# Kernel tuning notes

Hardware: AMD Instinct MI355X
Metric: run time of the kernel (lower is better)

## Reference

```python
import jax, jax.numpy as jnp
import numpy as np

DELTA = 10.0
EPS = 1e-08
THRESHOLD = 0.9
STEEPNESS = 10.0


def setup_inputs() -> dict:
    key = jax.random.key(0)
    k1, k2 = jax.random.split(key)
    B, T2, T1, F = 16, 2048, 512, 128
    mels = jax.random.normal(k1, (B, T2, F), dtype=jnp.float32)
    alpha = jax.random.uniform(k2, (B, T2, T1), dtype=jnp.float32)
    mel_mask = jnp.ones((B, T2), dtype=jnp.int32)
    text_mask = jnp.ones((B, T1), dtype=jnp.int32)
    return {"mels": mels, "alpha": alpha, "mel_mask": mel_mask, "text_mask": text_mask}


def reference(mels, alpha, mel_mask, text_mask):
    B, T2, F = mels.shape
    T1 = text_mask.shape[-1]
    audio_mask = mel_mask.astype(bool)
    txt_mask = text_mask.astype(bool)
    am_f = audio_mask.astype(alpha.dtype)  # [B, T2]
    tm_f = txt_mask.astype(alpha.dtype)    # [B, T1]

    # index vector p: [B, T1]
    p = jnp.broadcast_to(jnp.arange(T1, dtype=alpha.dtype), (B, T1))

    # cosine similarity between consecutive frames (F.normalize: x / max(||x||, 1e-12))
    norm = jnp.maximum(jnp.linalg.norm(mels, axis=-1, keepdims=True), 1e-12)
    z_norm = mels / norm
    cosine_sim = jnp.sum(z_norm[:, :-1] * z_norm[:, 1:], axis=-1)  # [B, T2-1]
    activity = jax.nn.sigmoid(STEEPNESS * (THRESHOLD - cosine_sim))
    activity = jnp.concatenate([jnp.ones((B, 1), dtype=activity.dtype), activity], axis=-1)
    activity = activity * am_f

    # soft monotonic index via gated cumsum of alpha-proposal increments
    imv_proposal = jnp.einsum('bts,bs->bt', alpha, p)  # [B, T2]
    delta_prop = jnp.concatenate(
        [jnp.zeros((B, 1), dtype=imv_proposal.dtype), jnp.diff(imv_proposal, axis=-1)], axis=-1)
    eff_delta = jnp.clip(delta_prop * activity, 0.0, 1.0)
    imv = jnp.cumsum(eff_delta, axis=-1) * am_f

    # rescale so last valid frame maps to last phoneme index
    last_idx = jnp.maximum(audio_mask.sum(-1).astype(jnp.int32) - 1, 0)  # [B]
    last_val = jnp.maximum(jnp.take_along_axis(imv, last_idx[:, None], axis=1)[:, 0], 1e-06)
    text_len = txt_mask.sum(-1).astype(imv.dtype)
    scale = jnp.maximum(text_len - 1.0, 0.0) / last_val
    imv = imv * scale[:, None] * am_f

    # gamma: masked softmax over phonemes of -delta * (imv - p)^2
    dist_sq = (imv[:, :, None] - p[:, None, :]) ** 2  # [B, T2, T1]
    logits = jnp.where(txt_mask[:, None, :], -DELTA * dist_sq, -1e9)
    gamma = jax.nn.softmax(logits, axis=-1) * am_f[:, :, None]

    # durations: soft mass per phoneme
    durations = jnp.sum(gamma * am_f[:, :, None], axis=1) * tm_f  # [B, T1]

    # attention-pooling of mel frames onto phonemes
    w = jnp.swapaxes(gamma, 1, 2) * am_f[:, None, :]  # [B, T1, T2]
    w = w / (jnp.sum(w, axis=-1, keepdims=True) + EPS)
    aligned_mels = jnp.einsum('bst,btf->bsf', w, mels) * tm_f[:, :, None]  # [B, T1, F]
    return aligned_mels, durations, imv
```

## Files before the change

kernel.cpp:

```cpp
#include <hip/hip_runtime.h>
#include <math.h>
#include <cstddef>

#define B_  16
#define T2_ 2048
#define T1_ 512
#define F_  128

constexpr float DELTA_C  = 10.0f;
constexpr float EPS_C    = 1e-8f;
constexpr float THRESH_C = 0.9f;
constexpr float STEEP_C  = 10.0f;

typedef float f4v __attribute__((ext_vector_type(4)));

__global__ __launch_bounds__(256) void actprop_kernel(const float* __restrict__ mels,
                                                      const float* __restrict__ alpha,
                                                      const int* __restrict__ mel_mask,
                                                      float* __restrict__ act,
                                                      float* __restrict__ prop) {
    int wid  = (int)((blockIdx.x * blockDim.x + threadIdx.x) >> 6);
    int lane = threadIdx.x & 63;
    if (wid >= B_ * T2_) return;
    int t = wid % T2_;

    const f4v* row = (const f4v*)(alpha + (size_t)wid * T1_);
    f4v v0 = __builtin_nontemporal_load(&row[lane]);
    f4v v1 = __builtin_nontemporal_load(&row[lane + 64]);

    float d = 0.f, n0 = 0.f, n1 = 0.f;
    if (t > 0) {
        float2 x = ((const float2*)(mels + (size_t)(wid - 1) * F_))[lane];
        float2 y = ((const float2*)(mels + (size_t)wid * F_))[lane];
        d  = x.x * y.x + x.y * y.y;
        n0 = x.x * x.x + x.y * x.y;
        n1 = y.x * y.x + y.y * y.y;
    }

    float fL = (float)(lane * 4);
    float psum = v0.x * fL + v0.y * (fL + 1.f) + v0.z * (fL + 2.f) + v0.w * (fL + 3.f)
               + v1.x * (fL + 256.f) + v1.y * (fL + 257.f) + v1.z * (fL + 258.f) + v1.w * (fL + 259.f);

    for (int off = 32; off > 0; off >>= 1) {
        psum += __shfl_xor(psum, off, 64);
        d    += __shfl_xor(d,    off, 64);
        n0   += __shfl_xor(n0,   off, 64);
        n1   += __shfl_xor(n1,   off, 64);
    }

    if (lane == 0) {
        float a_val;
        if (t == 0) {
            a_val = 1.0f;
        } else {
            float cs = d / (fmaxf(sqrtf(n0), 1e-12f) * fmaxf(sqrtf(n1), 1e-12f));
            a_val = 1.0f / (1.0f + __expf(-STEEP_C * (THRESH_C - cs)));
        }
        act[wid]  = a_val * (float)mel_mask[wid];
        prop[wid] = psum;
    }
}

__global__ __launch_bounds__(256) void scan_kernel(const float* __restrict__ prop,
                                                   const float* __restrict__ act,
                                                   const int* __restrict__ mel_mask,
                                                   const int* __restrict__ text_mask,
                                                   float* __restrict__ imv_out,
                                                   float2* __restrict__ packed,
                                                   int2* __restrict__ bounds) {
    int b    = blockIdx.x;
    int tid  = threadIdx.x;
    int wave = tid >> 6, lane = tid & 63;
    __shared__ float s_imv[T2_];
    __shared__ float s_wsum[4];
    __shared__ int   s_am4[4], s_tm4[4];
    __shared__ int   s_tm[T1_];

    const float* pr = prop + (size_t)b * T2_;
    const float* ac = act  + (size_t)b * T2_;
    const int*   mm = mel_mask  + (size_t)b * T2_;
    const int*   tm = text_mask + (size_t)b * T1_;

    int tmv0 = tm[tid], tmv1 = tm[tid + 256];
    s_tm[tid] = tmv0; s_tm[tid + 256] = tmv1;

    float e[8];
    int   mmv[8];
    int t0 = tid * 8;
    int am_local = 0;
    float run = 0.0f;
    for (int i = 0; i < 8; i++) {
        int t = t0 + i;
        float d = (t == 0) ? 0.0f : (pr[t] - pr[t - 1]) * ac[t];
        d = fminf(fmaxf(d, 0.0f), 1.0f);
        run += d;
        e[i] = run;
        mmv[i] = mm[t];
        am_local += mmv[i];
    }
    int tm_local = tmv0 + tmv1;
    for (int off = 32; off > 0; off >>= 1) {
        am_local += __shfl_xor(am_local, off, 64);
        tm_local += __shfl_xor(tm_local, off, 64);
    }
    if (lane == 0) { s_am4[wave] = am_local; s_tm4[wave] = tm_local; }

    float v = run;
    for (int off = 1; off < 64; off <<= 1) {
        float u = __shfl_up(v, off, 64);
        if (lane >= off) v += u;
    }
    if (lane == 63) s_wsum[wave] = v;
    __syncthreads();

    float woff = 0.0f;
    for (int w = 0; w < 4; w++) woff += (w < wave) ? s_wsum[w] : 0.0f;
    float excl = woff + v - run;
    for (int i = 0; i < 8; i++) {
        int t = t0 + i;
        s_imv[t] = (e[i] + excl) * (float)mmv[i];
    }
    __syncthreads();

    int am_total = s_am4[0] + s_am4[1] + s_am4[2] + s_am4[3];
    int tm_total = s_tm4[0] + s_tm4[1] + s_tm4[2] + s_tm4[3];
    int last_idx = max(am_total - 1, 0);
    float last_val = fmaxf(s_imv[last_idx], 1e-6f);
    float scale = fmaxf((float)tm_total - 1.0f, 0.0f) / last_val;
    __syncthreads();

    for (int i = 0; i < 8; i++) {
        int t = t0 + i;
        int valid = mmv[i];
        float vv = s_imv[t] * scale * (float)valid;
        imv_out[(size_t)b * T2_ + t] = vv;
        int c = (int)floorf(vv);
        float Z = 0.0f;
        for (int s = c - 2; s <= c + 3; s++) {
            if (s >= 0 && s < T1_ && s_tm[s]) {
                float dd = vv - (float)s;
                Z += __expf(-DELTA_C * dd * dd);
            }
        }
        Z = fmaxf(Z, 1e-30f);
        float key = valid ? vv : 3.0e4f;
        float2 pk = {key, valid ? (1.0f / Z) : 0.0f};
        packed[(size_t)b * T2_ + t] = pk;
        s_imv[t] = key;
    }
    __syncthreads();

    for (int k = 0; k < 2; k++) {
        int s = tid + k * 256;
        float lov = (float)s - 3.0f, hiv = (float)s + 3.0f;
        int lo = 0, hi = T2_;
        while (lo < hi) { int mid = (lo + hi) >> 1; if (s_imv[mid] >= lov) hi = mid; else lo = mid + 1; }
        int st = lo;
        hi = T2_;
        while (lo < hi) { int mid = (lo + hi) >> 1; if (s_imv[mid] > hiv) hi = mid; else lo = mid + 1; }
        int2 be = {st, lo};
        bounds[(size_t)b * T1_ + s] = be;
    }
}

__global__ __launch_bounds__(256) void pool_kernel(const float* __restrict__ mels,
                                                   const int* __restrict__ text_mask,
                                                   const float2* __restrict__ packed,
                                                   const int2* __restrict__ bounds,
                                                   float* __restrict__ aligned,
                                                   float* __restrict__ dur) {
    int wid  = (int)((blockIdx.x * blockDim.x + threadIdx.x) >> 6);
    int lane = threadIdx.x & 63;
    if (wid >= B_ * (T1_ / 2)) return;
    int b = wid >> 8, s0 = (wid & 255) * 2;
    float fs0 = (float)s0, fs1 = fs0 + 1.0f;

    const float2* pk   = packed + (size_t)b * T2_;
    const float2* mel2 = (const float2*)(mels + (size_t)b * T2_ * F_);
    int2 b0 = bounds[(size_t)b * T1_ + s0];
    int2 b1 = bounds[(size_t)b * T1_ + s0 + 1];
    int t_lo = b0.x, t_hi = b1.y;

    float ax0 = 0.f, ay0 = 0.f, g0s = 0.f;
    float ax1 = 0.f, ay1 = 0.f, g1s = 0.f;
    int t = t_lo;
    for (; t + 2 <= t_hi; t += 2) {
        float2 p0 = pk[t], p1 = pk[t + 1];
        float2 m0 = mel2[(size_t)t * 64 + lane];
        float2 m1 = mel2[(size_t)(t + 1) * 64 + lane];
        float d00 = p0.x - fs0, d01 = p0.x - fs1;
        float d10 = p1.x - fs0, d11 = p1.x - fs1;
        float g00 = __expf(-DELTA_C * d00 * d00) * p0.y;
        float g01 = __expf(-DELTA_C * d01 * d01) * p0.y;
        float g10 = __expf(-DELTA_C * d10 * d10) * p1.y;
        float g11 = __expf(-DELTA_C * d11 * d11) * p1.y;
        g0s += g00 + g10; g1s += g01 + g11;
        ax0 += g00 * m0.x + g10 * m1.x;  ay0 += g00 * m0.y + g10 * m1.y;
        ax1 += g01 * m0.x + g11 * m1.x;  ay1 += g01 * m0.y + g11 * m1.y;
    }
    for (; t < t_hi; t++) {
        float2 p = pk[t];
        float2 m = mel2[(size_t)t * 64 + lane];
        float d0 = p.x - fs0, d1 = p.x - fs1;
        float ga = __expf(-DELTA_C * d0 * d0) * p.y;
        float gb = __expf(-DELTA_C * d1 * d1) * p.y;
        g0s += ga; g1s += gb;
        ax0 += ga * m.x; ay0 += ga * m.y;
        ax1 += gb * m.x; ay1 += gb * m.y;
    }

    float tm0 = (float)text_mask[(size_t)b * T1_ + s0];
    float tm1 = (float)text_mask[(size_t)b * T1_ + s0 + 1];
    float inv0 = tm0 / (g0s + EPS_C);
    float inv1 = tm1 / (g1s + EPS_C);
    float2 o0 = {ax0 * inv0, ay0 * inv0};
    float2 o1 = {ax1 * inv1, ay1 * inv1};
    ((float2*)(aligned + ((size_t)b * T1_ + s0) * F_))[lane] = o0;
    ((float2*)(aligned + ((size_t)b * T1_ + s0 + 1) * F_))[lane] = o1;
    if (lane == 0) {
        dur[(size_t)b * T1_ + s0]     = g0s * tm0;
        dur[(size_t)b * T1_ + s0 + 1] = g1s * tm1;
    }
}

extern "C" void kernel_launch(void* const* d_in, const int* in_sizes, int n_in,
                              void* d_out, int out_size, void* d_ws, size_t ws_size,
                              hipStream_t stream) {
    const float* mels      = (const float*)d_in[0];
    const float* alpha     = (const float*)d_in[1];
    const int*   mel_mask  = (const int*)d_in[2];
    const int*   text_mask = (const int*)d_in[3];

    float* out     = (float*)d_out;
    float* aligned = out;
    float* dur     = out + (size_t)B_ * T1_ * F_;
    float* imv     = dur + (size_t)B_ * T1_;

    float*  ws     = (float*)d_ws;
    float*  act    = ws;
    float*  prop   = ws + (size_t)B_ * T2_;
    float2* packed = (float2*)(ws + 2 * (size_t)B_ * T2_);
    int2*   bounds = (int2*)(ws + 4 * (size_t)B_ * T2_);

    dim3 blk(256);
    actprop_kernel<<<(B_ * T2_) / 4, blk, 0, stream>>>(mels, alpha, mel_mask, act, prop);
    scan_kernel   <<<B_,            blk, 0, stream>>>(prop, act, mel_mask, text_mask, imv, packed, bounds);
    pool_kernel   <<<(B_ * T1_ / 2) / 4, blk, 0, stream>>>(mels, text_mask, packed, bounds, aligned, dur);
}
```

Before: 133.1 us.

## Fuse scan into pool kernel with redundant per-block scan recomputation

Merges the per-batch scan kernel into the pooling kernel: each of 64 blocks per batch recomputes the cumsum, scale and normalizers into shared memory, then pools 8 phonemes. This removes one launch, the 16-block serial scan stage and the global packed/bounds round trip. Act and prop are also packed into one float2 workspace array. The cost is 64x redundant scan work per batch and larger shared memory use.

New measurement: 134.4 us. Within noise of the previous version (+1.0%).

```diff
diff --git a/kernel.cpp b/kernel.cpp
--- a/kernel.cpp
+++ b/kernel.cpp
@@ -17,8 +17,7 @@
 __global__ __launch_bounds__(256) void actprop_kernel(const float* __restrict__ mels,
                                                       const float* __restrict__ alpha,
                                                       const int* __restrict__ mel_mask,
-                                                      float* __restrict__ act,
-                                                      float* __restrict__ prop) {
+                                                      float2* __restrict__ pa) {
     int wid  = (int)((blockIdx.x * blockDim.x + threadIdx.x) >> 6);
     int lane = threadIdx.x & 63;
     if (wid >= B_ * T2_) return;
@@ -56,30 +55,32 @@
             float cs = d / (fmaxf(sqrtf(n0), 1e-12f) * fmaxf(sqrtf(n1), 1e-12f));
             a_val = 1.0f / (1.0f + __expf(-STEEP_C * (THRESH_C - cs)));
         }
-        act[wid]  = a_val * (float)mel_mask[wid];
-        prop[wid] = psum;
+        float2 o = {psum, a_val * (float)mel_mask[wid]};
+        pa[wid] = o;
     }
 }
 
-__global__ __launch_bounds__(256) void scan_kernel(const float* __restrict__ prop,
-                                                   const float* __restrict__ act,
+__global__ __launch_bounds__(256) void pool_kernel(const float* __restrict__ mels,
+                                                   const float2* __restrict__ pa,
                                                    const int* __restrict__ mel_mask,
                                                    const int* __restrict__ text_mask,
                                                    float* __restrict__ imv_out,
-                                                   float2* __restrict__ packed,
-                                                   int2* __restrict__ bounds) {
-    int b    = blockIdx.x;
+                                                   float* __restrict__ aligned,
+                                                   float* __restrict__ dur) {
+    int bi   = blockIdx.x;
+    int b    = bi >> 6, sblk = bi & 63;
     int tid  = threadIdx.x;
     int wave = tid >> 6, lane = tid & 63;
-    __shared__ float s_imv[T2_];
+
+    __shared__ float s_key[T2_];
+    __shared__ float s_r[T2_];
     __shared__ float s_wsum[4];
     __shared__ int   s_am4[4], s_tm4[4];
     __shared__ int   s_tm[T1_];
 
-    const float* pr = prop + (size_t)b * T2_;
-    const float* ac = act  + (size_t)b * T2_;
-    const int*   mm = mel_mask  + (size_t)b * T2_;
-    const int*   tm = text_mask + (size_t)b * T1_;
+    const float2* pr = pa + (size_t)b * T2_;
+    const int*    mm = mel_mask  + (size_t)b * T2_;
+    const int*    tm = text_mask + (size_t)b * T1_;
 
     int tmv0 = tm[tid], tmv1 = tm[tid + 256];
     s_tm[tid] = tmv0; s_tm[tid + 256] = tmv1;
@@ -87,11 +88,14 @@
     float e[8];
     int   mmv[8];
     int t0 = tid * 8;
+    float prev = (t0 > 0) ? pr[t0 - 1].x : 0.0f;
+    float run = 0.0f;
     int am_local = 0;
-    float run = 0.0f;
     for (int i = 0; i < 8; i++) {
         int t = t0 + i;
-        float d = (t == 0) ? 0.0f : (pr[t] - pr[t - 1]) * ac[t];
+        float2 cur = pr[t];
+        float d = (t == 0) ? 0.0f : (cur.x - prev) * cur.y;
+        prev = cur.x;
         d = fminf(fmaxf(d, 0.0f), 1.0f);
         run += d;
         e[i] = run;
@@ -118,22 +122,22 @@
     float excl = woff + v - run;
     for (int i = 0; i < 8; i++) {
         int t = t0 + i;
-        s_imv[t] = (e[i] + excl) * (float)mmv[i];
+        s_key[t] = (e[i] + excl) * (float)mmv[i];
     }
     __syncthreads();
 
     int am_total = s_am4[0] + s_am4[1] + s_am4[2] + s_am4[3];
     int tm_total = s_tm4[0] + s_tm4[1] + s_tm4[2] + s_tm4[3];
     int last_idx = max(am_total - 1, 0);
-    float last_val = fmaxf(s_imv[last_idx], 1e-6f);
+    float last_val = fmaxf(s_key[last_idx], 1e-6f);
     float scale = fmaxf((float)tm_total - 1.0f, 0.0f) / last_val;
     __syncthreads();
 
     for (int i = 0; i < 8; i++) {
         int t = t0 + i;
         int valid = mmv[i];
-        float vv = s_imv[t] * scale * (float)valid;
-        imv_out[(size_t)b * T2_ + t] = vv;
+        float vv = s_key[t] * scale * (float)valid;
+        if (sblk == 0) imv_out[(size_t)b * T2_ + t] = vv;
         int c = (int)floorf(vv);
         float Z = 0.0f;
         for (int s = c - 2; s <= c + 3; s++) {
@@ -143,74 +147,54 @@
             }
         }
         Z = fmaxf(Z, 1e-30f);
-        float key = valid ? vv : 3.0e4f;
-        float2 pk = {key, valid ? (1.0f / Z) : 0.0f};
-        packed[(size_t)b * T2_ + t] = pk;
-        s_imv[t] = key;
-    }
-    __syncthreads();
-
-    for (int k = 0; k < 2; k++) {
-        int s = tid + k * 256;
-        float lov = (float)s - 3.0f, hiv = (float)s + 3.0f;
-        int lo = 0, hi = T2_;
-        while (lo < hi) { int mid = (lo + hi) >> 1; if (s_imv[mid] >= lov) hi = mid; else lo = mid + 1; }
-        int st = lo;
-        hi = T2_;
-        while (lo < hi) { int mid = (lo + hi) >> 1; if (s_imv[mid] > hiv) hi = mid; else lo = mid + 1; }
-        int2 be = {st, lo};
-        bounds[(size_t)b * T1_ + s] = be;
-    }
-}
-
-__global__ __launch_bounds__(256) void pool_kernel(const float* __restrict__ mels,
-                                                   const int* __restrict__ text_mask,
-                                                   const float2* __restrict__ packed,
-                                                   const int2* __restrict__ bounds,
-                                                   float* __restrict__ aligned,
-                                                   float* __restrict__ dur) {
-    int wid  = (int)((blockIdx.x * blockDim.x + threadIdx.x) >> 6);
-    int lane = threadIdx.x & 63;
-    if (wid >= B_ * (T1_ / 2)) return;
-    int b = wid >> 8, s0 = (wid & 255) * 2;
+        s_key[t] = valid ? vv : 3.0e4f;
+        s_r[t]   = valid ? (1.0f / Z) : 0.0f;
+    }
+    __syncthreads();
+
+    int s0 = sblk * 8 + wave * 2;
     float fs0 = (float)s0, fs1 = fs0 + 1.0f;
-
-    const float2* pk   = packed + (size_t)b * T2_;
     const float2* mel2 = (const float2*)(mels + (size_t)b * T2_ * F_);
-    int2 b0 = bounds[(size_t)b * T1_ + s0];
-    int2 b1 = bounds[(size_t)b * T1_ + s0 + 1];
-    int t_lo = b0.x, t_hi = b1.y;
+
+    float lov = fs0 - 3.0f, hiv = fs1 + 3.0f;
+    int lo = 0, hi = T2_;
+    while (lo < hi) { int mid = (lo + hi) >> 1; if (s_key[mid] >= lov) hi = mid; else lo = mid + 1; }
+    int t_lo = lo;
+    hi = T2_;
+    while (lo < hi) { int mid = (lo + hi) >> 1; if (s_key[mid] > hiv) hi = mid; else lo = mid + 1; }
+    int t_hi = lo;
 
     float ax0 = 0.f, ay0 = 0.f, g0s = 0.f;
     float ax1 = 0.f, ay1 = 0.f, g1s = 0.f;
     int t = t_lo;
     for (; t + 2 <= t_hi; t += 2) {
-        float2 p0 = pk[t], p1 = pk[t + 1];
+        float k0 = s_key[t], r0 = s_r[t];
+        float k1 = s_key[t + 1], r1 = s_r[t + 1];
         float2 m0 = mel2[(size_t)t * 64 + lane];
         float2 m1 = mel2[(size_t)(t + 1) * 64 + lane];
-        float d00 = p0.x - fs0, d01 = p0.x - fs1;
-        float d10 = p1.x - fs0, d11 = p1.x - fs1;
-        float g00 = __expf(-DELTA_C * d00 * d00) * p0.y;
-        float g01 = __expf(-DELTA_C * d01 * d01) * p0.y;
-        float g10 = __expf(-DELTA_C * d10 * d10) * p1.y;
-        float g11 = __expf(-DELTA_C * d11 * d11) * p1.y;
+        float d00 = k0 - fs0, d01 = k0 - fs1;
+        float d10 = k1 - fs0, d11 = k1 - fs1;
+        float g00 = __expf(-DELTA_C * d00 * d00) * r0;
+        float g01 = __expf(-DELTA_C * d01 * d01) * r0;
+        float g10 = __expf(-DELTA_C * d10 * d10) * r1;
+        float g11 = __expf(-DELTA_C * d11 * d11) * r1;
         g0s += g00 + g10; g1s += g01 + g11;
         ax0 += g00 * m0.x + g10 * m1.x;  ay0 += g00 * m0.y + g10 * m1.y;
         ax1 += g01 * m0.x + g11 * m1.x;  ay1 += g01 * m0.y + g11 * m1.y;
     }
     for (; t < t_hi; t++) {
-        float2 p = pk[t];
+        float k = s_key[t], r = s_r[t];
         float2 m = mel2[(size_t)t * 64 + lane];
-        float d0 = p.x - fs0, d1 = p.x - fs1;
-        float ga = __expf(-DELTA_C * d0 * d0) * p.y;
-        float gb = __expf(-DELTA_C * d1 * d1) * p.y;
+        float d0 = k - fs0, d1 = k - fs1;
+        float ga = __expf(-DELTA_C * d0 * d0) * r;
+        float gb = __expf(-DELTA_C * d1 * d1) * r;
         g0s += ga; g1s += gb;
         ax0 += ga * m.x; ay0 += ga * m.y;
         ax1 += gb * m.x; ay1 += gb * m.y;
     }
 
-    float tm0 = (float)text_mask[(size_t)b * T1_ + s0];
-    float tm1 = (float)text_mask[(size_t)b * T1_ + s0 + 1];
+    float tm0 = (float)s_tm[s0];
+    float tm1 = (float)s_tm[s0 + 1];
     float inv0 = tm0 / (g0s + EPS_C);
     float inv1 = tm1 / (g1s + EPS_C);
     float2 o0 = {ax0 * inv0, ay0 * inv0};
@@ -236,14 +220,9 @@
     float* dur     = out + (size_t)B_ * T1_ * F_;
     float* imv     = dur + (size_t)B_ * T1_;
 
-    float*  ws     = (float*)d_ws;
-    float*  act    = ws;
-    float*  prop   = ws + (size_t)B_ * T2_;
-    float2* packed = (float2*)(ws + 2 * (size_t)B_ * T2_);
-    int2*   bounds = (int2*)(ws + 4 * (size_t)B_ * T2_);
+    float2* pa = (float2*)d_ws;
 
     dim3 blk(256);
-    actprop_kernel<<<(B_ * T2_) / 4, blk, 0, stream>>>(mels, alpha, mel_mask, act, prop);
-    scan_kernel   <<<B_,            blk, 0, stream>>>(prop, act, mel_mask, text_mask, imv, packed, bounds);
-    pool_kernel   <<<(B_ * T1_ / 2) / 4, blk, 0, stream>>>(mels, text_mask, packed, bounds, aligned, dur);
+    actprop_kernel<<<(B_ * T2_) / 4, blk, 0, stream>>>(mels, alpha, mel_mask, pa);
+    pool_kernel   <<<B_ * 64,        blk, 0, stream>>>(mels, pa, mel_mask, text_mask, imv, aligned, dur);
 }
```
